# Kernel tuning notes

Measured on AMD Instinct MI355X. Metric: run time of the kernel, lower is better.

The kernel has to match this reference:

```python
import jax, jax.numpy as jnp
import numpy as np

TOP_K = 8
ROUTED_SCALING_FACTOR = 2.5
NORM_TOPK_PROB = True


def setup_inputs() -> dict:
    key = jax.random.key(0)
    k1, k2 = jax.random.split(key)
    hidden_states = jax.random.normal(k1, (4, 4096, 4096), dtype=jnp.float32)
    # gate weight: (n_routed_experts, hidden_size)
    weight = jax.random.normal(k2, (256, 4096), dtype=jnp.float32) * (1.0 / np.sqrt(4096))
    return {"hidden_states": hidden_states, "weight": weight}


def reference(hidden_states, weight):
    bsz, seq_len, h = hidden_states.shape
    x = hidden_states.reshape(-1, h).astype(jnp.float32)  # [T, h]
    # gate logits: [T, E]
    logits = jnp.einsum("th,eh->te", x, weight.astype(jnp.float32))
    scores = jax.nn.softmax(logits, axis=-1)
    topk_weight, topk_idx = jax.lax.top_k(scores, TOP_K)  # [T, k]
    if TOP_K > 1 and NORM_TOPK_PROB:
        denom = jnp.sum(topk_weight, axis=-1, keepdims=True) + 1e-20
        topk_weight = topk_weight / denom * ROUTED_SCALING_FACTOR
    else:
        topk_weight = topk_weight * ROUTED_SCALING_FACTOR
    return (topk_idx, topk_weight)
```

## Files before the change

kernel.cpp:

```cpp
#include <hip/hip_runtime.h>
#include <math.h>

typedef _Float16 half8  __attribute__((ext_vector_type(8)));
typedef _Float16 half4v __attribute__((ext_vector_type(4)));
typedef float    f32x16 __attribute__((ext_vector_type(16)));

namespace {
constexpr int H      = 4096;
constexpr int E      = 256;
constexpr int TOPK   = 8;
constexpr int NCAND  = 12;
constexpr int BM     = 64;
constexpr int BK     = 32;
constexpr int NCHUNK = H / BK;
constexpr int SLD    = E + 4;
constexpr float DELTA = 5e-4f;
constexpr size_t WF_BYTES = (size_t)E * H * 2 * 2;
constexpr int SMEM_BYTES = BM * SLD * 4;
}

__global__ void convert_w_kernel(const float* __restrict__ W,
                                 _Float16* __restrict__ Wf) {
    int t  = blockIdx.x * blockDim.x + threadIdx.x;
    int e  = t >> 10;
    int kq = t & 1023;
    float4 w4 = *(const float4*)(W + ((size_t)e << 12) + (kq << 2));
    float x0 = w4.x * 64.0f, x1 = w4.y * 64.0f, x2 = w4.z * 64.0f, x3 = w4.w * 64.0f;
    _Float16 h0 = (_Float16)x0, h1 = (_Float16)x1, h2 = (_Float16)x2, h3 = (_Float16)x3;
    _Float16 l0 = (_Float16)(x0 - (float)h0), l1 = (_Float16)(x1 - (float)h1);
    _Float16 l2 = (_Float16)(x2 - (float)h2), l3 = (_Float16)(x3 - (float)h3);
    int k    = kq << 2;
    int nt   = e >> 5;
    int ks   = k >> 4;
    int lane = (e & 31) | (((k >> 3) & 1) << 5);
    int j    = k & 7;
    size_t base = (((size_t)nt * 256 + ks) * 2) * 512 + lane * 8 + j;
    half4v hv = {h0, h1, h2, h3};
    half4v lv = {l0, l1, l2, l3};
    *(half4v*)(Wf + base)       = hv;
    *(half4v*)(Wf + base + 512) = lv;
}

struct BF { half8 h[2][2]; half8 l[2][2]; };

__global__ __launch_bounds__(512, 2)
void moe_gate_mfma(const float* __restrict__ X, const _Float16* __restrict__ Wf,
                   const float* __restrict__ Wg,
                   float* __restrict__ out_idx, float* __restrict__ out_w) {
    __shared__ __align__(16) char smem[SMEM_BYTES];
    _Float16* Abuf = (_Float16*)smem;
    float*    sc   = (float*)smem;

    const int tid  = threadIdx.x;
    const int lane = tid & 63;
    const int wave = tid >> 6;
    const int wr   = wave >> 2;
    const int wc   = wave & 3;
    const int m0   = blockIdx.x * BM;

    const int m_s  = tid >> 3;
    const int kq_s = tid & 7;
    const int ks_s = kq_s >> 2;
    const int mt_s = m_s >> 5;
    const int ln_s = (m_s & 31) | (((kq_s >> 1) & 1) << 5);
    const int j_s  = (kq_s & 1) * 4;
    const int dst_s = ((ks_s * 2 + mt_s) * 2) * 512 + ln_s * 8 + j_s;
    const float* xgp = X + (size_t)(m0 + m_s) * H + kq_s * 4;

    f32x16 acc[2];
    #pragma unroll
    for (int nt = 0; nt < 2; ++nt)
        #pragma unroll
        for (int r = 0; r < 16; ++r) acc[nt][r] = 0.0f;

    auto load_b = [&](int kc, BF& b) {
        #pragma unroll
        for (int ks = 0; ks < 2; ++ks)
            #pragma unroll
            for (int nt = 0; nt < 2; ++nt) {
                size_t base = (((size_t)(2 * wc + nt) * 256 + (kc * 2 + ks)) * 2) * 512
                              + lane * 8;
                b.h[ks][nt] = *(const half8*)(Wf + base);
                b.l[ks][nt] = *(const half8*)(Wf + base + 512);
            }
    };
    auto stage = [&](int bufIdx, float4 xv) {
        _Float16* buf = Abuf + bufIdx * 4096;
        float x0 = xv.x, x1 = xv.y, x2 = xv.z, x3 = xv.w;
        _Float16 h0 = (_Float16)x0, h1 = (_Float16)x1, h2 = (_Float16)x2, h3 = (_Float16)x3;
        _Float16 l0 = (_Float16)(x0 - (float)h0), l1 = (_Float16)(x1 - (float)h1);
        _Float16 l2 = (_Float16)(x2 - (float)h2), l3 = (_Float16)(x3 - (float)h3);
        half4v hv = {h0, h1, h2, h3};
        half4v lv = {l0, l1, l2, l3};
        *(half4v*)(buf + dst_s)       = hv;
        *(half4v*)(buf + dst_s + 512) = lv;
    };
    auto compute = [&](int bufIdx, const BF& b) {
        const _Float16* buf = Abuf + bufIdx * 4096;
        #pragma unroll
        for (int ks = 0; ks < 2; ++ks) {
            const _Float16* p = buf + (ks * 2 + wr) * 1024 + lane * 8;
            half8 a_hi = *(const half8*)p;
            half8 a_lo = *(const half8*)(p + 512);
            #pragma unroll
            for (int nt = 0; nt < 2; ++nt) {
                acc[nt] = __builtin_amdgcn_mfma_f32_32x32x16_f16(a_hi, b.h[ks][nt], acc[nt], 0, 0, 0);
                acc[nt] = __builtin_amdgcn_mfma_f32_32x32x16_f16(a_lo, b.h[ks][nt], acc[nt], 0, 0, 0);
                acc[nt] = __builtin_amdgcn_mfma_f32_32x32x16_f16(a_hi, b.l[ks][nt], acc[nt], 0, 0, 0);
            }
        }
    };

    BF bcur;
    load_b(0, bcur);
    float4 xv = *(const float4*)(xgp);
    stage(0, xv);
    __syncthreads();
    float4 xnxt = *(const float4*)(xgp + BK);

    for (int kc = 0; kc < NCHUNK; ++kc) {
        BF bnxt;
        float4 xfar = make_float4(0.f, 0.f, 0.f, 0.f);
        if (kc + 1 < NCHUNK) load_b(kc + 1, bnxt);
        if (kc + 2 < NCHUNK) xfar = *(const float4*)(xgp + (size_t)(kc + 2) * BK);
        compute(kc & 1, bcur);
        if (kc + 1 < NCHUNK) {
            stage((kc + 1) & 1, xnxt);
            __syncthreads();
        }
        bcur = bnxt;
        xnxt = xfar;
    }

    __syncthreads();
    #pragma unroll
    for (int nt = 0; nt < 2; ++nt) {
        #pragma unroll
        for (int r = 0; r < 16; ++r) {
            int row = (r & 3) + 8 * (r >> 2) + 4 * (lane >> 5);
            int col = lane & 31;
            sc[(wr * 32 + row) * SLD + wc * 64 + nt * 32 + col] = acc[nt][r] * 0.015625f;
        }
    }
    __syncthreads();

    for (int t8 = 0; t8 < 8; ++t8) {
        const int t = wave * 8 + t8;
        float4 pv = *(const float4*)(sc + t * SLD + lane * 4);
        float p0 = pv.x, p1 = pv.y, p2 = pv.z, p3 = pv.w;

        float tv[NCAND]; int ti[NCAND];
        #pragma unroll
        for (int s = 0; s < NCAND; ++s) {
            float bv = p0; int bi = lane * 4;
            if (p1 > bv || (p1 == bv && lane * 4 + 1 < bi)) { bv = p1; bi = lane * 4 + 1; }
            if (p2 > bv || (p2 == bv && lane * 4 + 2 < bi)) { bv = p2; bi = lane * 4 + 2; }
            if (p3 > bv || (p3 == bv && lane * 4 + 3 < bi)) { bv = p3; bi = lane * 4 + 3; }
            #pragma unroll
            for (int off = 32; off > 0; off >>= 1) {
                float ov = __shfl_xor(bv, off, 64);
                int   oi = __shfl_xor(bi, off, 64);
                if (ov > bv || (ov == bv && oi < bi)) { bv = ov; bi = oi; }
            }
            tv[s] = bv; ti[s] = bi;
            if ((bi >> 2) == lane) {
                const int sl = bi & 3;
                if      (sl == 0) p0 = -3e38f;
                else if (sl == 1) p1 = -3e38f;
                else if (sl == 2) p2 = -3e38f;
                else              p3 = -3e38f;
            }
        }

        bool rescue = false;
        #pragma unroll
        for (int g = 0; g < 9; ++g) rescue |= (tv[g] - tv[g + 1] < DELTA);

        if (rescue) {
            double dv[NCAND];
            const float* xr = X + (size_t)(m0 + t) * H;
            #pragma unroll 1
            for (int c = 0; c < NCAND; ++c) {
                const float* wrow = Wg + (size_t)ti[c] * H;
                double s_ = 0.0;
                #pragma unroll
                for (int it = 0; it < 16; ++it) {
                    float4 xa = *(const float4*)(xr + it * 256 + lane * 4);
                    float4 wa = *(const float4*)(wrow + it * 256 + lane * 4);
                    s_ += (double)xa.x * wa.x + (double)xa.y * wa.y
                        + (double)xa.z * wa.z + (double)xa.w * wa.w;
                }
                #pragma unroll
                for (int off = 32; off > 0; off >>= 1) s_ += __shfl_xor(s_, off, 64);
                dv[c] = s_;
            }
            int si[NCAND];
            #pragma unroll
            for (int c = 0; c < NCAND; ++c) si[c] = ti[c];
            #pragma unroll
            for (int a = 0; a < TOPK; ++a) {
                int best = a;
                #pragma unroll
                for (int b = a + 1; b < NCAND; ++b) {
                    if (dv[b] > dv[best] || (dv[b] == dv[best] && si[b] < si[best])) best = b;
                }
                double tdv = dv[a]; dv[a] = dv[best]; dv[best] = tdv;
                int    tsi = si[a]; si[a] = si[best]; si[best] = tsi;
            }
            #pragma unroll
            for (int s = 0; s < TOPK; ++s) { tv[s] = (float)dv[s]; ti[s] = si[s]; }
        }

        if (lane == 0) {
            float M = tv[0];
            float e8[TOPK]; float den = 0.0f;
            #pragma unroll
            for (int s = 0; s < TOPK; ++s) { e8[s] = expf(tv[s] - M); den += e8[s]; }
            float scl = 2.5f / den;
            size_t tok = (size_t)(m0 + t);
            #pragma unroll
            for (int s = 0; s < TOPK; ++s) {
                out_idx[tok * TOPK + s] = (float)ti[s];
                out_w[tok * TOPK + s]   = e8[s] * scl;
            }
        }
    }
}

namespace fb {
constexpr int BM = 32, BK = 32;
constexpr int XS_LD = BM + 4, WS_LD = E + 4;
constexpr int LDS_FLOATS = BK * XS_LD + BK * WS_LD;
}

__global__ __launch_bounds__(256, 2)
void moe_gate_fallback(const float* __restrict__ X, const float* __restrict__ W,
                       float* __restrict__ out_idx, float* __restrict__ out_w) {
    __shared__ float lds[fb::LDS_FLOATS];
    float* xs = lds;
    float* ws = lds + fb::BK * fb::XS_LD;
    const int tid = threadIdx.x;
    const int tx = tid & 31, ty = tid >> 5;
    const int m0 = blockIdx.x * fb::BM;
    float acc[4][8];
    #pragma unroll
    for (int i = 0; i < 4; ++i)
        #pragma unroll
        for (int j = 0; j < 8; ++j) acc[i][j] = 0.0f;
    const int lr = tid >> 3, lc = (tid & 7) * 4;
    const float* xg = X + (size_t)(m0 + lr) * H + lc;
    const float* wg = W + (size_t)lr * H + lc;
    for (int kc = 0; kc < H; kc += fb::BK) {
        float4 xv = *(const float4*)(xg + kc);
        float4 wv[8];
        #pragma unroll
        for (int i = 0; i < 8; ++i) wv[i] = *(const float4*)(wg + (size_t)i * 32 * H + kc);
        __syncthreads();
        #pragma unroll
        for (int j = 0; j < 4; ++j) xs[(lc + j) * fb::XS_LD + lr] = ((const float*)&xv)[j];
        #pragma unroll
        for (int i = 0; i < 8; ++i)
            #pragma unroll
            for (int j = 0; j < 4; ++j)
                ws[(lc + j) * fb::WS_LD + i * 32 + lr] = ((const float*)&wv[i])[j];
        __syncthreads();
        #pragma unroll
        for (int kk = 0; kk < fb::BK; ++kk) {
            float4 xa = *(const float4*)(xs + kk * fb::XS_LD + ty * 4);
            float4 wb0 = *(const float4*)(ws + kk * fb::WS_LD + tx * 8);
            float4 wb1 = *(const float4*)(ws + kk * fb::WS_LD + tx * 8 + 4);
            const float xr[4] = {xa.x, xa.y, xa.z, xa.w};
            const float wr8[8] = {wb0.x, wb0.y, wb0.z, wb0.w, wb1.x, wb1.y, wb1.z, wb1.w};
            #pragma unroll
            for (int i = 0; i < 4; ++i)
                #pragma unroll
                for (int j = 0; j < 8; ++j) acc[i][j] = fmaf(xr[i], wr8[j], acc[i][j]);
        }
    }
    __syncthreads();
    float* sc = lds;
    #pragma unroll
    for (int i = 0; i < 4; ++i) {
        *(float4*)(sc + (ty * 4 + i) * fb::WS_LD + tx * 8) =
            make_float4(acc[i][0], acc[i][1], acc[i][2], acc[i][3]);
        *(float4*)(sc + (ty * 4 + i) * fb::WS_LD + tx * 8 + 4) =
            make_float4(acc[i][4], acc[i][5], acc[i][6], acc[i][7]);
    }
    __syncthreads();
    const int wave = tid >> 6, lane = tid & 63;
    for (int t8 = 0; t8 < 8; ++t8) {
        const int t = wave * 8 + t8;
        float4 pv = *(const float4*)(sc + t * fb::WS_LD + lane * 4);
        float v0 = pv.x, v1 = pv.y, v2 = pv.z, v3 = pv.w;
        float M = fmaxf(fmaxf(v0, v1), fmaxf(v2, v3));
        #pragma unroll
        for (int off = 32; off > 0; off >>= 1) M = fmaxf(M, __shfl_xor(M, off, 64));
        float p0 = expf(v0 - M), p1 = expf(v1 - M), p2 = expf(v2 - M), p3 = expf(v3 - M);
        float z = p0 + p1 + p2 + p3;
        #pragma unroll
        for (int off = 32; off > 0; off >>= 1) z += __shfl_xor(z, off, 64);
        p0 /= z; p1 /= z; p2 /= z; p3 /= z;
        float tv[TOPK]; int ti[TOPK];
        #pragma unroll
        for (int s = 0; s < TOPK; ++s) {
            float bv = p0; int bi = lane * 4;
            if (p1 > bv || (p1 == bv && lane * 4 + 1 < bi)) { bv = p1; bi = lane * 4 + 1; }
            if (p2 > bv || (p2 == bv && lane * 4 + 2 < bi)) { bv = p2; bi = lane * 4 + 2; }
            if (p3 > bv || (p3 == bv && lane * 4 + 3 < bi)) { bv = p3; bi = lane * 4 + 3; }
            #pragma unroll
            for (int off = 32; off > 0; off >>= 1) {
                float ov = __shfl_xor(bv, off, 64);
                int   oi = __shfl_xor(bi, off, 64);
                if (ov > bv || (ov == bv && oi < bi)) { bv = ov; bi = oi; }
            }
            tv[s] = bv; ti[s] = bi;
            if ((bi >> 2) == lane) {
                const int sl = bi & 3;
                if      (sl == 0) p0 = -1.0f;
                else if (sl == 1) p1 = -1.0f;
                else if (sl == 2) p2 = -1.0f;
                else              p3 = -1.0f;
            }
        }
        if (lane == 0) {
            float den = tv[0] + tv[1] + tv[2] + tv[3] + tv[4] + tv[5] + tv[6] + tv[7] + 1e-20f;
            float scl = 2.5f / den;
            size_t tok = (size_t)(m0 + t);
            #pragma unroll
            for (int s = 0; s < TOPK; ++s) {
                out_idx[tok * TOPK + s] = (float)ti[s];
                out_w[tok * TOPK + s]   = tv[s] * scl;
            }
        }
    }
}

extern "C" void kernel_launch(void* const* d_in, const int* in_sizes, int n_in,
                              void* d_out, int out_size, void* d_ws, size_t ws_size,
                              hipStream_t stream) {
    const float* X = (const float*)d_in[0];
    const float* W = (const float*)d_in[1];
    float* out = (float*)d_out;
    const int T = in_sizes[0] / H;
    float* out_idx = out;
    float* out_w   = out + (size_t)T * TOPK;

    if (ws_size >= WF_BYTES && (T % BM) == 0) {
        _Float16* Wf = (_Float16*)d_ws;
        hipLaunchKernelGGL(convert_w_kernel, dim3((E * (H / 4)) / 256), dim3(256), 0, stream, W, Wf);
        hipLaunchKernelGGL(moe_gate_mfma, dim3(T / BM), dim3(512), 0, stream, X, Wf, W, out_idx, out_w);
    } else {
        hipLaunchKernelGGL(moe_gate_fallback, dim3(T / fb::BM), dim3(256), 0, stream, X, W, out_idx, out_w);
    }
}
```

Before: 691.5 us.

## Load A fragments directly from global into registers, drop LDS staging and syncs

Each wave now loads its X fragments directly from global memory into MFMA register layout and converts them to hi/lo fp16 in registers, removing the LDS staging buffer and the per-chunk __syncthreads. The block grows to 1024 threads (16 waves), each owning one 32x32 output tile instead of two. A two-stage register pipeline prefetches the weight and X fragments. The cost is that each X row is re-read by the 8 waves covering different expert columns, relying on cache, and register pressure rises under launch_bounds(1024,4).

```diff
diff --git a/kernel.cpp b/kernel.cpp
--- a/kernel.cpp
+++ b/kernel.cpp
@@ -3,6 +3,7 @@
 
 typedef _Float16 half8  __attribute__((ext_vector_type(8)));
 typedef _Float16 half4v __attribute__((ext_vector_type(4)));
+typedef __fp16   fp16x2 __attribute__((ext_vector_type(2)));
 typedef float    f32x16 __attribute__((ext_vector_type(16)));
 
 namespace {
@@ -16,7 +17,6 @@
 constexpr int SLD    = E + 4;
 constexpr float DELTA = 5e-4f;
 constexpr size_t WF_BYTES = (size_t)E * H * 2 * 2;
-constexpr int SMEM_BYTES = BM * SLD * 4;
 }
 
 __global__ void convert_w_kernel(const float* __restrict__ W,
@@ -41,121 +41,94 @@
     *(half4v*)(Wf + base + 512) = lv;
 }
 
-struct BF { half8 h[2][2]; half8 l[2][2]; };
-
-__global__ __launch_bounds__(512, 2)
+struct Pipe { half8 bh[2], bl[2]; float4 a[2][2]; };
+
+__global__ __launch_bounds__(1024, 4)
 void moe_gate_mfma(const float* __restrict__ X, const _Float16* __restrict__ Wf,
                    const float* __restrict__ Wg,
                    float* __restrict__ out_idx, float* __restrict__ out_w) {
-    __shared__ __align__(16) char smem[SMEM_BYTES];
-    _Float16* Abuf = (_Float16*)smem;
-    float*    sc   = (float*)smem;
+    __shared__ float sc[BM * SLD];
 
     const int tid  = threadIdx.x;
     const int lane = tid & 63;
     const int wave = tid >> 6;
-    const int wr   = wave >> 2;
-    const int wc   = wave & 3;
+    const int mt   = wave >> 3;
+    const int wc   = wave & 7;
     const int m0   = blockIdx.x * BM;
 
-    const int m_s  = tid >> 3;
-    const int kq_s = tid & 7;
-    const int ks_s = kq_s >> 2;
-    const int mt_s = m_s >> 5;
-    const int ln_s = (m_s & 31) | (((kq_s >> 1) & 1) << 5);
-    const int j_s  = (kq_s & 1) * 4;
-    const int dst_s = ((ks_s * 2 + mt_s) * 2) * 512 + ln_s * 8 + j_s;
-    const float* xgp = X + (size_t)(m0 + m_s) * H + kq_s * 4;
-
-    f32x16 acc[2];
+    const int arow = lane & 31;
+    const int akhi = (lane >> 5) << 3;
+    const float* xrow = X + (size_t)(m0 + mt * 32 + arow) * H + akhi;
+    const _Float16* wbase = Wf + (size_t)wc * 256 * 2 * 512 + (size_t)lane * 8;
+
+    f32x16 acc;
     #pragma unroll
-    for (int nt = 0; nt < 2; ++nt)
-        #pragma unroll
-        for (int r = 0; r < 16; ++r) acc[nt][r] = 0.0f;
-
-    auto load_b = [&](int kc, BF& b) {
-        #pragma unroll
-        for (int ks = 0; ks < 2; ++ks)
-            #pragma unroll
-            for (int nt = 0; nt < 2; ++nt) {
-                size_t base = (((size_t)(2 * wc + nt) * 256 + (kc * 2 + ks)) * 2) * 512
-                              + lane * 8;
-                b.h[ks][nt] = *(const half8*)(Wf + base);
-                b.l[ks][nt] = *(const half8*)(Wf + base + 512);
-            }
+    for (int r = 0; r < 16; ++r) acc[r] = 0.0f;
+
+    auto load_pipe = [&](int kc, Pipe& P) {
+        #pragma unroll
+        for (int ks = 0; ks < 2; ++ks) {
+            size_t off = (size_t)(kc * 2 + ks) * 1024;
+            P.bh[ks]   = *(const half8*)(wbase + off);
+            P.bl[ks]   = *(const half8*)(wbase + off + 512);
+            P.a[ks][0] = *(const float4*)(xrow + kc * 32 + ks * 16);
+            P.a[ks][1] = *(const float4*)(xrow + kc * 32 + ks * 16 + 4);
+        }
     };
-    auto stage = [&](int bufIdx, float4 xv) {
-        _Float16* buf = Abuf + bufIdx * 4096;
-        float x0 = xv.x, x1 = xv.y, x2 = xv.z, x3 = xv.w;
-        _Float16 h0 = (_Float16)x0, h1 = (_Float16)x1, h2 = (_Float16)x2, h3 = (_Float16)x3;
-        _Float16 l0 = (_Float16)(x0 - (float)h0), l1 = (_Float16)(x1 - (float)h1);
-        _Float16 l2 = (_Float16)(x2 - (float)h2), l3 = (_Float16)(x3 - (float)h3);
-        half4v hv = {h0, h1, h2, h3};
-        half4v lv = {l0, l1, l2, l3};
-        *(half4v*)(buf + dst_s)       = hv;
-        *(half4v*)(buf + dst_s + 512) = lv;
+    auto compute = [&](const Pipe& P) {
+        #pragma unroll
+        for (int ks = 0; ks < 2; ++ks) {
+            const float4 u = P.a[ks][0], v = P.a[ks][1];
+            fp16x2 h0 = __builtin_amdgcn_cvt_pkrtz(u.x, u.y);
+            fp16x2 h1 = __builtin_amdgcn_cvt_pkrtz(u.z, u.w);
+            fp16x2 h2 = __builtin_amdgcn_cvt_pkrtz(v.x, v.y);
+            fp16x2 h3 = __builtin_amdgcn_cvt_pkrtz(v.z, v.w);
+            fp16x2 l0 = __builtin_amdgcn_cvt_pkrtz(u.x - (float)h0.x, u.y - (float)h0.y);
+            fp16x2 l1 = __builtin_amdgcn_cvt_pkrtz(u.z - (float)h1.x, u.w - (float)h1.y);
+            fp16x2 l2 = __builtin_amdgcn_cvt_pkrtz(v.x - (float)h2.x, v.y - (float)h2.y);
+            fp16x2 l3 = __builtin_amdgcn_cvt_pkrtz(v.z - (float)h3.x, v.w - (float)h3.y);
+            half8 ah = {(_Float16)h0.x, (_Float16)h0.y, (_Float16)h1.x, (_Float16)h1.y,
+                        (_Float16)h2.x, (_Float16)h2.y, (_Float16)h3.x, (_Float16)h3.y};
+            half8 al = {(_Float16)l0.x, (_Float16)l0.y, (_Float16)l1.x, (_Float16)l1.y,
+                        (_Float16)l2.x, (_Float16)l2.y, (_Float16)l3.x, (_Float16)l3.y};
+            acc = __builtin_amdgcn_mfma_f32_32x32x16_f16(ah, P.bh[ks], acc, 0, 0, 0);
+            acc = __builtin_amdgcn_mfma_f32_32x32x16_f16(al, P.bh[ks], acc, 0, 0, 0);
+            acc = __builtin_amdgcn_mfma_f32_32x32x16_f16(ah, P.bl[ks], acc, 0, 0, 0);
+        }
     };
-    auto compute = [&](int bufIdx, const BF& b) {
-        const _Float16* buf = Abuf + bufIdx * 4096;
-        #pragma unroll
-        for (int ks = 0; ks < 2; ++ks) {
-            const _Float16* p = buf + (ks * 2 + wr) * 1024 + lane * 8;
-            half8 a_hi = *(const half8*)p;
-            half8 a_lo = *(const half8*)(p + 512);
-            #pragma unroll
-            for (int nt = 0; nt < 2; ++nt) {
-                acc[nt] = __builtin_amdgcn_mfma_f32_32x32x16_f16(a_hi, b.h[ks][nt], acc[nt], 0, 0, 0);
-                acc[nt] = __builtin_amdgcn_mfma_f32_32x32x16_f16(a_lo, b.h[ks][nt], acc[nt], 0, 0, 0);
-                acc[nt] = __builtin_amdgcn_mfma_f32_32x32x16_f16(a_hi, b.l[ks][nt], acc[nt], 0, 0, 0);
-            }
-        }
-    };
-
-    BF bcur;
-    load_b(0, bcur);
-    float4 xv = *(const float4*)(xgp);
-    stage(0, xv);
+
+    Pipe p0, p1;
+    load_pipe(0, p0);
+    #pragma unroll 1
+    for (int kc = 0; kc < NCHUNK; kc += 2) {
+        const int k1 = kc + 1;
+        const int k2 = (kc + 2 < NCHUNK) ? kc + 2 : kc;
+        load_pipe(k1, p1);
+        compute(p0);
+        load_pipe(k2, p0);
+        compute(p1);
+    }
+
+    #pragma unroll
+    for (int r = 0; r < 16; ++r) {
+        int row = (r & 3) + 8 * (r >> 2) + 4 * (lane >> 5);
+        int col = lane & 31;
+        sc[(mt * 32 + row) * SLD + wc * 32 + col] = acc[r] * 0.015625f;
+    }
     __syncthreads();
-    float4 xnxt = *(const float4*)(xgp + BK);
-
-    for (int kc = 0; kc < NCHUNK; ++kc) {
-        BF bnxt;
-        float4 xfar = make_float4(0.f, 0.f, 0.f, 0.f);
-        if (kc + 1 < NCHUNK) load_b(kc + 1, bnxt);
-        if (kc + 2 < NCHUNK) xfar = *(const float4*)(xgp + (size_t)(kc + 2) * BK);
-        compute(kc & 1, bcur);
-        if (kc + 1 < NCHUNK) {
-            stage((kc + 1) & 1, xnxt);
-            __syncthreads();
-        }
-        bcur = bnxt;
-        xnxt = xfar;
-    }
-
-    __syncthreads();
-    #pragma unroll
-    for (int nt = 0; nt < 2; ++nt) {
-        #pragma unroll
-        for (int r = 0; r < 16; ++r) {
-            int row = (r & 3) + 8 * (r >> 2) + 4 * (lane >> 5);
-            int col = lane & 31;
-            sc[(wr * 32 + row) * SLD + wc * 64 + nt * 32 + col] = acc[nt][r] * 0.015625f;
-        }
-    }
-    __syncthreads();
-
-    for (int t8 = 0; t8 < 8; ++t8) {
-        const int t = wave * 8 + t8;
+
+    for (int t4 = 0; t4 < 4; ++t4) {
+        const int t = wave * 4 + t4;
         float4 pv = *(const float4*)(sc + t * SLD + lane * 4);
-        float p0 = pv.x, p1 = pv.y, p2 = pv.z, p3 = pv.w;
+        float p0s = pv.x, p1s = pv.y, p2s = pv.z, p3s = pv.w;
 
         float tv[NCAND]; int ti[NCAND];
         #pragma unroll
         for (int s = 0; s < NCAND; ++s) {
-            float bv = p0; int bi = lane * 4;
-            if (p1 > bv || (p1 == bv && lane * 4 + 1 < bi)) { bv = p1; bi = lane * 4 + 1; }
-            if (p2 > bv || (p2 == bv && lane * 4 + 2 < bi)) { bv = p2; bi = lane * 4 + 2; }
-            if (p3 > bv || (p3 == bv && lane * 4 + 3 < bi)) { bv = p3; bi = lane * 4 + 3; }
+            float bv = p0s; int bi = lane * 4;
+            if (p1s > bv || (p1s == bv && lane * 4 + 1 < bi)) { bv = p1s; bi = lane * 4 + 1; }
+            if (p2s > bv || (p2s == bv && lane * 4 + 2 < bi)) { bv = p2s; bi = lane * 4 + 2; }
+            if (p3s > bv || (p3s == bv && lane * 4 + 3 < bi)) { bv = p3s; bi = lane * 4 + 3; }
             #pragma unroll
             for (int off = 32; off > 0; off >>= 1) {
                 float ov = __shfl_xor(bv, off, 64);
@@ -165,10 +138,10 @@
             tv[s] = bv; ti[s] = bi;
             if ((bi >> 2) == lane) {
                 const int sl = bi & 3;
-                if      (sl == 0) p0 = -3e38f;
-                else if (sl == 1) p1 = -3e38f;
-                else if (sl == 2) p2 = -3e38f;
-                else              p3 = -3e38f;
+                if      (sl == 0) p0s = -3e38f;
+                else if (sl == 1) p1s = -3e38f;
+                else if (sl == 2) p2s = -3e38f;
+                else              p3s = -3e38f;
             }
         }
 
@@ -348,7 +321,7 @@
     if (ws_size >= WF_BYTES && (T % BM) == 0) {
         _Float16* Wf = (_Float16*)d_ws;
         hipLaunchKernelGGL(convert_w_kernel, dim3((E * (H / 4)) / 256), dim3(256), 0, stream, W, Wf);
-        hipLaunchKernelGGL(moe_gate_mfma, dim3(T / BM), dim3(512), 0, stream, X, Wf, W, out_idx, out_w);
+        hipLaunchKernelGGL(moe_gate_mfma, dim3(T / BM), dim3(1024), 0, stream, X, Wf, W, out_idx, out_w);
     } else {
         hipLaunchKernelGGL(moe_gate_fallback, dim3(T / fb::BM), dim3(256), 0, stream, X, W, out_idx, out_w);
     }
```

After: 908.1 us. 31.3% more time.

## Shrink token tile to 32 rows with one 32-expert column per wave

Applied to the files above, without the earlier changes.

Halves the block's token tile from 64 to 32 rows. The 8 waves now each own a single 32-expert column group instead of a 2x4 grid with two n-tiles each, and only half the threads stage X into shared memory. This doubles the grid and lowers per-wave accumulator and B-register pressure, which may improve occupancy and latency hiding. The cost is that each weight fragment is reused across half as many tokens, doubling weight traffic from L2, and there are fewer MFMAs per B load.

```diff
diff --git a/kernel.cpp b/kernel.cpp
--- a/kernel.cpp
+++ b/kernel.cpp
@@ -10,7 +10,7 @@
 constexpr int E      = 256;
 constexpr int TOPK   = 8;
 constexpr int NCAND  = 12;
-constexpr int BM     = 64;
+constexpr int BM     = 32;
 constexpr int BK     = 32;
 constexpr int NCHUNK = H / BK;
 constexpr int SLD    = E + 4;
@@ -30,18 +30,18 @@
     _Float16 l0 = (_Float16)(x0 - (float)h0), l1 = (_Float16)(x1 - (float)h1);
     _Float16 l2 = (_Float16)(x2 - (float)h2), l3 = (_Float16)(x3 - (float)h3);
     int k    = kq << 2;
-    int nt   = e >> 5;
+    int grp  = e >> 5;
     int ks   = k >> 4;
     int lane = (e & 31) | (((k >> 3) & 1) << 5);
     int j    = k & 7;
-    size_t base = (((size_t)nt * 256 + ks) * 2) * 512 + lane * 8 + j;
+    size_t base = (((size_t)grp * 256 + ks) * 2) * 512 + lane * 8 + j;
     half4v hv = {h0, h1, h2, h3};
     half4v lv = {l0, l1, l2, l3};
     *(half4v*)(Wf + base)       = hv;
     *(half4v*)(Wf + base + 512) = lv;
 }
 
-struct BF { half8 h[2][2]; half8 l[2][2]; };
+struct BF { half8 h[2]; half8 l[2]; };
 
 __global__ __launch_bounds__(512, 2)
 void moe_gate_mfma(const float* __restrict__ X, const _Float16* __restrict__ Wf,
@@ -54,38 +54,33 @@
     const int tid  = threadIdx.x;
     const int lane = tid & 63;
     const int wave = tid >> 6;
-    const int wr   = wave >> 2;
-    const int wc   = wave & 3;
+    const int wc   = wave;
     const int m0   = blockIdx.x * BM;
 
-    const int m_s  = tid >> 3;
+    const bool active = tid < 256;
+    const int m_s  = (tid >> 3) & 31;
     const int kq_s = tid & 7;
     const int ks_s = kq_s >> 2;
-    const int mt_s = m_s >> 5;
-    const int ln_s = (m_s & 31) | (((kq_s >> 1) & 1) << 5);
+    const int ln_s = m_s | (((kq_s >> 1) & 1) << 5);
     const int j_s  = (kq_s & 1) * 4;
-    const int dst_s = ((ks_s * 2 + mt_s) * 2) * 512 + ln_s * 8 + j_s;
+    const int dst_s = ks_s * 1024 + ln_s * 8 + j_s;
     const float* xgp = X + (size_t)(m0 + m_s) * H + kq_s * 4;
 
-    f32x16 acc[2];
+    f32x16 acc;
     #pragma unroll
-    for (int nt = 0; nt < 2; ++nt)
-        #pragma unroll
-        for (int r = 0; r < 16; ++r) acc[nt][r] = 0.0f;
+    for (int r = 0; r < 16; ++r) acc[r] = 0.0f;
 
     auto load_b = [&](int kc, BF& b) {
         #pragma unroll
-        for (int ks = 0; ks < 2; ++ks)
-            #pragma unroll
-            for (int nt = 0; nt < 2; ++nt) {
-                size_t base = (((size_t)(2 * wc + nt) * 256 + (kc * 2 + ks)) * 2) * 512
-                              + lane * 8;
-                b.h[ks][nt] = *(const half8*)(Wf + base);
-                b.l[ks][nt] = *(const half8*)(Wf + base + 512);
-            }
+        for (int ks = 0; ks < 2; ++ks) {
+            size_t base = (((size_t)wc * 256 + (kc * 2 + ks)) * 2) * 512 + lane * 8;
+            b.h[ks] = *(const half8*)(Wf + base);
+            b.l[ks] = *(const half8*)(Wf + base + 512);
+        }
     };
     auto stage = [&](int bufIdx, float4 xv) {
-        _Float16* buf = Abuf + bufIdx * 4096;
+        if (!active) return;
+        _Float16* buf = Abuf + bufIdx * 2048;
         float x0 = xv.x, x1 = xv.y, x2 = xv.z, x3 = xv.w;
         _Float16 h0 = (_Float16)x0, h1 = (_Float16)x1, h2 = (_Float16)x2, h3 = (_Float16)x3;
         _Float16 l0 = (_Float16)(x0 - (float)h0), l1 = (_Float16)(x1 - (float)h1);
@@ -96,18 +91,15 @@
         *(half4v*)(buf + dst_s + 512) = lv;
     };
     auto compute = [&](int bufIdx, const BF& b) {
-        const _Float16* buf = Abuf + bufIdx * 4096;
+        const _Float16* buf = Abuf + bufIdx * 2048;
         #pragma unroll
         for (int ks = 0; ks < 2; ++ks) {
-            const _Float16* p = buf + (ks * 2 + wr) * 1024 + lane * 8;
+            const _Float16* p = buf + ks * 1024 + lane * 8;
             half8 a_hi = *(const half8*)p;
             half8 a_lo = *(const half8*)(p + 512);
-            #pragma unroll
-            for (int nt = 0; nt < 2; ++nt) {
-                acc[nt] = __builtin_amdgcn_mfma_f32_32x32x16_f16(a_hi, b.h[ks][nt], acc[nt], 0, 0, 0);
-                acc[nt] = __builtin_amdgcn_mfma_f32_32x32x16_f16(a_lo, b.h[ks][nt], acc[nt], 0, 0, 0);
-                acc[nt] = __builtin_amdgcn_mfma_f32_32x32x16_f16(a_hi, b.l[ks][nt], acc[nt], 0, 0, 0);
-            }
+            acc = __builtin_amdgcn_mfma_f32_32x32x16_f16(a_hi, b.h[ks], acc, 0, 0, 0);
+            acc = __builtin_amdgcn_mfma_f32_32x32x16_f16(a_lo, b.h[ks], acc, 0, 0, 0);
+            acc = __builtin_amdgcn_mfma_f32_32x32x16_f16(a_hi, b.l[ks], acc, 0, 0, 0);
         }
     };
 
@@ -134,18 +126,15 @@
 
     __syncthreads();
     #pragma unroll
-    for (int nt = 0; nt < 2; ++nt) {
-        #pragma unroll
-        for (int r = 0; r < 16; ++r) {
-            int row = (r & 3) + 8 * (r >> 2) + 4 * (lane >> 5);
-            int col = lane & 31;
-            sc[(wr * 32 + row) * SLD + wc * 64 + nt * 32 + col] = acc[nt][r] * 0.015625f;
-        }
-    }
-    __syncthreads();
-
-    for (int t8 = 0; t8 < 8; ++t8) {
-        const int t = wave * 8 + t8;
+    for (int r = 0; r < 16; ++r) {
+        int row = (r & 3) + 8 * (r >> 2) + 4 * (lane >> 5);
+        int col = lane & 31;
+        sc[row * SLD + wc * 32 + col] = acc[r] * 0.015625f;
+    }
+    __syncthreads();
+
+    for (int t4 = 0; t4 < 4; ++t4) {
+        const int t = wave * 4 + t4;
         float4 pv = *(const float4*)(sc + t * SLD + lane * 4);
         float p0 = pv.x, p1 = pv.y, p2 = pv.z, p3 = pv.w;
 
```

Result: slower. 750.9 us (+8.6%).

## Enlarge MFMA block tile to 256 tokens to reuse weight fragments across four M-tiles

Applied to the files above, without the earlier changes.

Each block now covers 256 tokens instead of 64, and each wave accumulates four 32-row M-tiles against the same B fragments. This cuts global weight reads per token by a factor of four. The cost is a 64KB LDS double buffer, 128 accumulator floats per lane and launch bounds lowered to one block per CU. Weight prefetching across chunks is dropped, so B loads are issued in the same iteration they are used. The epilogue now writes scores and runs top-k in four 64-token passes through shared memory.

```diff
diff --git a/kernel.cpp b/kernel.cpp
--- a/kernel.cpp
+++ b/kernel.cpp
@@ -10,13 +10,13 @@
 constexpr int E      = 256;
 constexpr int TOPK   = 8;
 constexpr int NCAND  = 12;
-constexpr int BM     = 64;
+constexpr int BM     = 256;
 constexpr int BK     = 32;
 constexpr int NCHUNK = H / BK;
-constexpr int SLD    = E + 4;
+constexpr int SLD    = 256;
 constexpr float DELTA = 5e-4f;
 constexpr size_t WF_BYTES = (size_t)E * H * 2 * 2;
-constexpr int SMEM_BYTES = BM * SLD * 4;
+constexpr int SMEM_BYTES = 65536;
 }
 
 __global__ void convert_w_kernel(const float* __restrict__ W,
@@ -30,20 +30,21 @@
     _Float16 l0 = (_Float16)(x0 - (float)h0), l1 = (_Float16)(x1 - (float)h1);
     _Float16 l2 = (_Float16)(x2 - (float)h2), l3 = (_Float16)(x3 - (float)h3);
     int k    = kq << 2;
-    int nt   = e >> 5;
+    int grp  = e >> 5;
     int ks   = k >> 4;
     int lane = (e & 31) | (((k >> 3) & 1) << 5);
     int j    = k & 7;
-    size_t base = (((size_t)nt * 256 + ks) * 2) * 512 + lane * 8 + j;
+    size_t base = (((size_t)grp * 256 + ks) * 2) * 512 + lane * 8 + j;
     half4v hv = {h0, h1, h2, h3};
     half4v lv = {l0, l1, l2, l3};
     *(half4v*)(Wf + base)       = hv;
     *(half4v*)(Wf + base + 512) = lv;
 }
 
-struct BF { half8 h[2][2]; half8 l[2][2]; };
-
-__global__ __launch_bounds__(512, 2)
+struct BReg { half8 h[2][2], l[2][2]; };
+struct X4   { float4 v[4]; };
+
+__global__ __launch_bounds__(512, 1)
 void moe_gate_mfma(const float* __restrict__ X, const _Float16* __restrict__ Wf,
                    const float* __restrict__ Wg,
                    float* __restrict__ out_idx, float* __restrict__ out_w) {
@@ -54,176 +55,201 @@
     const int tid  = threadIdx.x;
     const int lane = tid & 63;
     const int wave = tid >> 6;
-    const int wr   = wave >> 2;
+    const int mr   = wave >> 2;
     const int wc   = wave & 3;
     const int m0   = blockIdx.x * BM;
 
-    const int m_s  = tid >> 3;
-    const int kq_s = tid & 7;
-    const int ks_s = kq_s >> 2;
-    const int mt_s = m_s >> 5;
-    const int ln_s = (m_s & 31) | (((kq_s >> 1) & 1) << 5);
-    const int j_s  = (kq_s & 1) * 4;
-    const int dst_s = ((ks_s * 2 + mt_s) * 2) * 512 + ln_s * 8 + j_s;
-    const float* xgp = X + (size_t)(m0 + m_s) * H + kq_s * 4;
-
-    f32x16 acc[2];
-    #pragma unroll
-    for (int nt = 0; nt < 2; ++nt)
-        #pragma unroll
-        for (int r = 0; r < 16; ++r) acc[nt][r] = 0.0f;
-
-    auto load_b = [&](int kc, BF& b) {
+    const int q_tid3 = tid >> 3;
+    const int kq_s   = tid & 7;
+    const int ks_s   = kq_s >> 2;
+    const int j_s    = (kq_s & 1) * 4;
+    const int lane_s = (q_tid3 & 31) | (((kq_s >> 1) & 1) << 5);
+    int dst_q[4];
+    const float* xg_q[4];
+    #pragma unroll
+    for (int q = 0; q < 4; ++q) {
+        const int mt = (q_tid3 >> 5) + 2 * q;
+        dst_q[q] = ((ks_s * 8 + mt) * 2) * 512 + lane_s * 8 + j_s;
+        xg_q[q]  = X + (size_t)(m0 + q_tid3 + 64 * q) * H + kq_s * 4;
+    }
+
+    const _Float16* wbase = Wf + (size_t)lane * 8;
+
+    f32x16 acc[4][2];
+    #pragma unroll
+    for (int tl = 0; tl < 4; ++tl)
+        #pragma unroll
+        for (int nt = 0; nt < 2; ++nt)
+            #pragma unroll
+            for (int r = 0; r < 16; ++r) acc[tl][nt][r] = 0.0f;
+
+    auto load_x = [&](int kc) {
+        X4 x;
+        #pragma unroll
+        for (int q = 0; q < 4; ++q) x.v[q] = *(const float4*)(xg_q[q] + kc * BK);
+        return x;
+    };
+    auto stage = [&](int bufIdx, const X4& x) {
+        _Float16* buf = Abuf + bufIdx * 16384;
+        #pragma unroll
+        for (int q = 0; q < 4; ++q) {
+            float x0 = x.v[q].x, x1 = x.v[q].y, x2 = x.v[q].z, x3 = x.v[q].w;
+            _Float16 h0 = (_Float16)x0, h1 = (_Float16)x1,
+                     h2 = (_Float16)x2, h3 = (_Float16)x3;
+            _Float16 l0 = (_Float16)(x0 - (float)h0), l1 = (_Float16)(x1 - (float)h1);
+            _Float16 l2 = (_Float16)(x2 - (float)h2), l3 = (_Float16)(x3 - (float)h3);
+            half4v hv = {h0, h1, h2, h3};
+            half4v lv = {l0, l1, l2, l3};
+            *(half4v*)(buf + dst_q[q])       = hv;
+            *(half4v*)(buf + dst_q[q] + 512) = lv;
+        }
+    };
+    auto load_b = [&](int kc, BReg& b) {
+        #pragma unroll
+        for (int nt = 0; nt < 2; ++nt)
+            #pragma unroll
+            for (int ks = 0; ks < 2; ++ks) {
+                size_t base = (((size_t)(2 * wc + nt) * 256 + (kc * 2 + ks)) * 2) * 512;
+                b.h[nt][ks] = *(const half8*)(wbase + base);
+                b.l[nt][ks] = *(const half8*)(wbase + base + 512);
+            }
+    };
+    auto compute = [&](int bufIdx, const BReg& b) {
+        const _Float16* buf = Abuf + bufIdx * 16384;
         #pragma unroll
         for (int ks = 0; ks < 2; ++ks)
             #pragma unroll
-            for (int nt = 0; nt < 2; ++nt) {
-                size_t base = (((size_t)(2 * wc + nt) * 256 + (kc * 2 + ks)) * 2) * 512
-                              + lane * 8;
-                b.h[ks][nt] = *(const half8*)(Wf + base);
-                b.l[ks][nt] = *(const half8*)(Wf + base + 512);
+            for (int tl = 0; tl < 4; ++tl) {
+                const _Float16* p = buf + ((ks * 8 + (mr * 4 + tl)) * 2) * 512 + lane * 8;
+                half8 a_hi = *(const half8*)p;
+                half8 a_lo = *(const half8*)(p + 512);
+                #pragma unroll
+                for (int nt = 0; nt < 2; ++nt) {
+                    acc[tl][nt] = __builtin_amdgcn_mfma_f32_32x32x16_f16(a_hi, b.h[nt][ks], acc[tl][nt], 0, 0, 0);
+                    acc[tl][nt] = __builtin_amdgcn_mfma_f32_32x32x16_f16(a_lo, b.h[nt][ks], acc[tl][nt], 0, 0, 0);
+                    acc[tl][nt] = __builtin_amdgcn_mfma_f32_32x32x16_f16(a_hi, b.l[nt][ks], acc[tl][nt], 0, 0, 0);
+                }
             }
     };
-    auto stage = [&](int bufIdx, float4 xv) {
-        _Float16* buf = Abuf + bufIdx * 4096;
-        float x0 = xv.x, x1 = xv.y, x2 = xv.z, x3 = xv.w;
-        _Float16 h0 = (_Float16)x0, h1 = (_Float16)x1, h2 = (_Float16)x2, h3 = (_Float16)x3;
-        _Float16 l0 = (_Float16)(x0 - (float)h0), l1 = (_Float16)(x1 - (float)h1);
-        _Float16 l2 = (_Float16)(x2 - (float)h2), l3 = (_Float16)(x3 - (float)h3);
-        half4v hv = {h0, h1, h2, h3};
-        half4v lv = {l0, l1, l2, l3};
-        *(half4v*)(buf + dst_s)       = hv;
-        *(half4v*)(buf + dst_s + 512) = lv;
-    };
-    auto compute = [&](int bufIdx, const BF& b) {
-        const _Float16* buf = Abuf + bufIdx * 4096;
-        #pragma unroll
-        for (int ks = 0; ks < 2; ++ks) {
-            const _Float16* p = buf + (ks * 2 + wr) * 1024 + lane * 8;
-            half8 a_hi = *(const half8*)p;
-            half8 a_lo = *(const half8*)(p + 512);
-            #pragma unroll
-            for (int nt = 0; nt < 2; ++nt) {
-                acc[nt] = __builtin_amdgcn_mfma_f32_32x32x16_f16(a_hi, b.h[ks][nt], acc[nt], 0, 0, 0);
-                acc[nt] = __builtin_amdgcn_mfma_f32_32x32x16_f16(a_lo, b.h[ks][nt], acc[nt], 0, 0, 0);
-                acc[nt] = __builtin_amdgcn_mfma_f32_32x32x16_f16(a_hi, b.l[ks][nt], acc[nt], 0, 0, 0);
-            }
-        }
-    };
-
-    BF bcur;
-    load_b(0, bcur);
-    float4 xv = *(const float4*)(xgp);
-    stage(0, xv);
+
+    {
+        X4 x0v = load_x(0);
+        stage(0, x0v);
+    }
     __syncthreads();
-    float4 xnxt = *(const float4*)(xgp + BK);
-
+
+    #pragma unroll 1
     for (int kc = 0; kc < NCHUNK; ++kc) {
-        BF bnxt;
-        float4 xfar = make_float4(0.f, 0.f, 0.f, 0.f);
-        if (kc + 1 < NCHUNK) load_b(kc + 1, bnxt);
-        if (kc + 2 < NCHUNK) xfar = *(const float4*)(xgp + (size_t)(kc + 2) * BK);
-        compute(kc & 1, bcur);
-        if (kc + 1 < NCHUNK) {
-            stage((kc + 1) & 1, xnxt);
-            __syncthreads();
-        }
-        bcur = bnxt;
-        xnxt = xfar;
-    }
-
-    __syncthreads();
-    #pragma unroll
-    for (int nt = 0; nt < 2; ++nt) {
-        #pragma unroll
-        for (int r = 0; r < 16; ++r) {
-            int row = (r & 3) + 8 * (r >> 2) + 4 * (lane >> 5);
-            int col = lane & 31;
-            sc[(wr * 32 + row) * SLD + wc * 64 + nt * 32 + col] = acc[nt][r] * 0.015625f;
-        }
-    }
-    __syncthreads();
-
-    for (int t8 = 0; t8 < 8; ++t8) {
-        const int t = wave * 8 + t8;
-        float4 pv = *(const float4*)(sc + t * SLD + lane * 4);
-        float p0 = pv.x, p1 = pv.y, p2 = pv.z, p3 = pv.w;
-
-        float tv[NCAND]; int ti[NCAND];
-        #pragma unroll
-        for (int s = 0; s < NCAND; ++s) {
-            float bv = p0; int bi = lane * 4;
-            if (p1 > bv || (p1 == bv && lane * 4 + 1 < bi)) { bv = p1; bi = lane * 4 + 1; }
-            if (p2 > bv || (p2 == bv && lane * 4 + 2 < bi)) { bv = p2; bi = lane * 4 + 2; }
-            if (p3 > bv || (p3 == bv && lane * 4 + 3 < bi)) { bv = p3; bi = lane * 4 + 3; }
-            #pragma unroll
-            for (int off = 32; off > 0; off >>= 1) {
-                float ov = __shfl_xor(bv, off, 64);
-                int   oi = __shfl_xor(bi, off, 64);
-                if (ov > bv || (ov == bv && oi < bi)) { bv = ov; bi = oi; }
-            }
-            tv[s] = bv; ti[s] = bi;
-            if ((bi >> 2) == lane) {
-                const int sl = bi & 3;
-                if      (sl == 0) p0 = -3e38f;
-                else if (sl == 1) p1 = -3e38f;
-                else if (sl == 2) p2 = -3e38f;
-                else              p3 = -3e38f;
-            }
-        }
-
-        bool rescue = false;
-        #pragma unroll
-        for (int g = 0; g < 9; ++g) rescue |= (tv[g] - tv[g + 1] < DELTA);
-
-        if (rescue) {
-            double dv[NCAND];
-            const float* xr = X + (size_t)(m0 + t) * H;
-            #pragma unroll 1
-            for (int c = 0; c < NCAND; ++c) {
-                const float* wrow = Wg + (size_t)ti[c] * H;
-                double s_ = 0.0;
-                #pragma unroll
-                for (int it = 0; it < 16; ++it) {
-                    float4 xa = *(const float4*)(xr + it * 256 + lane * 4);
-                    float4 wa = *(const float4*)(wrow + it * 256 + lane * 4);
-                    s_ += (double)xa.x * wa.x + (double)xa.y * wa.y
-                        + (double)xa.z * wa.z + (double)xa.w * wa.w;
-                }
-                #pragma unroll
-                for (int off = 32; off > 0; off >>= 1) s_ += __shfl_xor(s_, off, 64);
-                dv[c] = s_;
-            }
-            int si[NCAND];
-            #pragma unroll
-            for (int c = 0; c < NCAND; ++c) si[c] = ti[c];
-            #pragma unroll
-            for (int a = 0; a < TOPK; ++a) {
-                int best = a;
-                #pragma unroll
-                for (int b = a + 1; b < NCAND; ++b) {
-                    if (dv[b] > dv[best] || (dv[b] == dv[best] && si[b] < si[best])) best = b;
-                }
-                double tdv = dv[a]; dv[a] = dv[best]; dv[best] = tdv;
-                int    tsi = si[a]; si[a] = si[best]; si[best] = tsi;
-            }
-            #pragma unroll
-            for (int s = 0; s < TOPK; ++s) { tv[s] = (float)dv[s]; ti[s] = si[s]; }
-        }
-
-        if (lane == 0) {
-            float M = tv[0];
-            float e8[TOPK]; float den = 0.0f;
-            #pragma unroll
-            for (int s = 0; s < TOPK; ++s) { e8[s] = expf(tv[s] - M); den += e8[s]; }
-            float scl = 2.5f / den;
-            size_t tok = (size_t)(m0 + t);
-            #pragma unroll
-            for (int s = 0; s < TOPK; ++s) {
-                out_idx[tok * TOPK + s] = (float)ti[s];
-                out_w[tok * TOPK + s]   = e8[s] * scl;
-            }
-        }
+        BReg b;
+        load_b(kc, b);
+        X4 xn;
+        if (kc + 1 < NCHUNK) xn = load_x(kc + 1);
+        compute(kc & 1, b);
+        if (kc + 1 < NCHUNK) stage((kc + 1) & 1, xn);
+        __syncthreads();
+    }
+
+    #pragma unroll
+    for (int p = 0; p < 4; ++p) {
+        if (mr == (p >> 1)) {
+            #pragma unroll
+            for (int s = 0; s < 2; ++s) {
+                const int tl = (p & 1) * 2 + s;
+                #pragma unroll
+                for (int nt = 0; nt < 2; ++nt)
+                    #pragma unroll
+                    for (int r = 0; r < 16; ++r) {
+                        int row = (r & 3) + 8 * (r >> 2) + 4 * (lane >> 5);
+                        int col = lane & 31;
+                        sc[(s * 32 + row) * SLD + wc * 64 + nt * 32 + col] =
+                            acc[tl][nt][r] * 0.015625f;
+                    }
+            }
+        }
+        __syncthreads();
+
+        for (int t8 = 0; t8 < 8; ++t8) {
+            const int t   = wave * 8 + t8;
+            const int tok = m0 + p * 64 + t;
+            float4 pv = *(const float4*)(sc + t * SLD + lane * 4);
+            float p0 = pv.x, p1 = pv.y, p2 = pv.z, p3 = pv.w;
+
+            float tv[NCAND]; int ti[NCAND];
+            #pragma unroll
+            for (int s = 0; s < NCAND; ++s) {
+                float bv = p0; int bi = lane * 4;
+                if (p1 > bv || (p1 == bv && lane * 4 + 1 < bi)) { bv = p1; bi = lane * 4 + 1; }
+                if (p2 > bv || (p2 == bv && lane * 4 + 2 < bi)) { bv = p2; bi = lane * 4 + 2; }
+                if (p3 > bv || (p3 == bv && lane * 4 + 3 < bi)) { bv = p3; bi = lane * 4 + 3; }
+                #pragma unroll
+                for (int off = 32; off > 0; off >>= 1) {
+                    float ov = __shfl_xor(bv, off, 64);
+                    int   oi = __shfl_xor(bi, off, 64);
+                    if (ov > bv || (ov == bv && oi < bi)) { bv = ov; bi = oi; }
+                }
+                tv[s] = bv; ti[s] = bi;
+                if ((bi >> 2) == lane) {
+                    const int sl = bi & 3;
+                    if      (sl == 0) p0 = -3e38f;
+                    else if (sl == 1) p1 = -3e38f;
+                    else if (sl == 2) p2 = -3e38f;
+                    else              p3 = -3e38f;
+                }
+            }
+
+            bool rescue = false;
+            #pragma unroll
+            for (int g = 0; g < 9; ++g) rescue |= (tv[g] - tv[g + 1] < DELTA);
+
+            if (rescue) {
+                double dv[NCAND];
+                const float* xr = X + (size_t)tok * H;
+                #pragma unroll 1
+                for (int c = 0; c < NCAND; ++c) {
+                    const float* wrow = Wg + (size_t)ti[c] * H;
+                    double s_ = 0.0;
+                    #pragma unroll
+                    for (int it = 0; it < 16; ++it) {
+                        float4 xa = *(const float4*)(xr + it * 256 + lane * 4);
+                        float4 wa = *(const float4*)(wrow + it * 256 + lane * 4);
+                        s_ += (double)xa.x * wa.x + (double)xa.y * wa.y
+                            + (double)xa.z * wa.z + (double)xa.w * wa.w;
+                    }
+                    #pragma unroll
+                    for (int off = 32; off > 0; off >>= 1) s_ += __shfl_xor(s_, off, 64);
+                    dv[c] = s_;
+                }
+                int si[NCAND];
+                #pragma unroll
+                for (int c = 0; c < NCAND; ++c) si[c] = ti[c];
+                #pragma unroll
+                for (int a = 0; a < TOPK; ++a) {
+                    int best = a;
+                    #pragma unroll
+                    for (int b2 = a + 1; b2 < NCAND; ++b2) {
+                        if (dv[b2] > dv[best] || (dv[b2] == dv[best] && si[b2] < si[best])) best = b2;
+                    }
+                    double tdv = dv[a]; dv[a] = dv[best]; dv[best] = tdv;
+                    int    tsi = si[a]; si[a] = si[best]; si[best] = tsi;
+                }
+                #pragma unroll
+                for (int s = 0; s < TOPK; ++s) { tv[s] = (float)dv[s]; ti[s] = si[s]; }
+            }
+
+            if (lane == 0) {
+                float M = tv[0];
+                float e8[TOPK]; float den = 0.0f;
+                #pragma unroll
+                for (int s = 0; s < TOPK; ++s) { e8[s] = expf(tv[s] - M); den += e8[s]; }
+                float scl = 2.5f / den;
+                #pragma unroll
+                for (int s = 0; s < TOPK; ++s) {
+                    out_idx[(size_t)tok * TOPK + s] = (float)ti[s];
+                    out_w[(size_t)tok * TOPK + s]   = e8[s] * scl;
+                }
+            }
+        }
+        __syncthreads();
     }
 }
 
```

Result: slower. 1.282 ms (+85.5%).
